# Optimization experiments

Hardware: AMD Instinct MI355X
Metric: run time of the kernel (lower is better)

## Reference

```python
import jax, jax.numpy as jnp
import numpy as np

EPS = 1e-8


def setup_inputs() -> dict:
    key = jax.random.key(0)
    k1, k2, k3, k4 = jax.random.split(key, 4)
    N, D, P, H = 8192, 512, 128, 128
    x1 = jax.random.normal(k1, (N, D), dtype=jnp.float32)
    proj_w1 = jax.random.normal(k2, (D, D), dtype=jnp.float32) * (1.0 / np.sqrt(D))
    proj_w2 = jax.random.normal(k3, (D, P), dtype=jnp.float32) * (1.0 / np.sqrt(D))
    gc_w = jax.random.normal(k4, (D, H), dtype=jnp.float32) * (1.0 / np.sqrt(D))
    gc_b = jnp.zeros((H,), dtype=jnp.float32)
    return {"x1": x1, "proj_w1": proj_w1, "proj_w2": proj_w2, "gc_w": gc_w, "gc_b": gc_b}


def _cosine_similarity(x):
    # torch.mm(x, x.T) / clamp(||x|| * ||x||.T, eps)
    w = jnp.sqrt(jnp.sum(x * x, axis=1, keepdims=True))  # [N,1]
    return (x @ x.T) / jnp.maximum(w * w.T, EPS)


def reference(x1, proj_w1, proj_w2, gc_w, gc_b):
    # projector: Linear(512,512,bias=False) -> ReLU -> Linear(512,P,bias=False)
    x_proj = jax.nn.relu(x1 @ proj_w1) @ proj_w2  # [N,P]
    # graph build is under @torch.no_grad(): dense fully-connected weighted graph
    A = jax.lax.stop_gradient(_cosine_similarity(x_proj))  # [N,N]
    N = x1.shape[0]
    # WGraphConv (DGL GraphConv w/ edge weights, norm='both'):
    # fully connected graph incl. self loops -> in_degree = N, norm = N^{-1/2} on both sides
    inv_n = jnp.asarray(1.0 / N, dtype=x1.dtype)
    h = x1 @ gc_w            # project first (D > H, cheaper)  [N,H]
    h = (A @ h) * inv_n      # weighted aggregate, symmetric degree norm
    return h + gc_b          # [N,H]
```

## Files before the change

kernel.cpp:

```cpp
#include <hip/hip_runtime.h>
#include <stdint.h>
#include <stddef.h>

typedef short s16x4 __attribute__((ext_vector_type(4)));
typedef short s16x8 __attribute__((ext_vector_type(8)));
typedef float f32x4 __attribute__((ext_vector_type(4)));

#define NN 8192
#define DD 512
#define PP 128
#define HH 128

__device__ __forceinline__ short f2bf(float f) {
  unsigned u = __builtin_bit_cast(unsigned, f);
  u = (u + 0x7fffu + ((u >> 16) & 1u)) >> 16;
  return (short)u;
}

__device__ __forceinline__ void async16(const void* g, void* l) {
  __builtin_amdgcn_global_load_lds(
      (const __attribute__((address_space(1))) unsigned int*)g,
      (__attribute__((address_space(3))) unsigned int*)l, 16, 0, 0);
}

template <int MF>
__device__ __forceinline__ void gemm_core(
    const short* __restrict__ A, long lda,
    const short* __restrict__ BT, long ldb,
    long rowBase, long colBase, int k0, int k1,
    short* As, short* Bs, f32x4 (*acc)[4]) {
  const int tid  = threadIdx.x;
  const int lane = tid & 63;
  const int wid  = tid >> 6;
  const int wr   = (wid >> 1) * (MF * 16);
  const int wc   = (wid & 1) * 64;
  const int srow = lane >> 3;
  const int skk  = (lane & 7) * 8;

  for (int k = k0; k < k1; k += 64) {
#pragma unroll
    for (int it = 0; it < MF; ++it) {
      int r = wid * (MF * 8) + it * 8;
      async16(A + (rowBase + r + srow) * lda + k + skk, As + r * 64);
    }
#pragma unroll
    for (int it = 0; it < 4; ++it) {
      int r = wid * 32 + it * 8;
      async16(BT + (colBase + r + srow) * ldb + k + skk, Bs + r * 64);
    }
    __syncthreads();
#pragma unroll
    for (int ks = 0; ks < 64; ks += 32) {
      s16x8 af[MF], bfv[4];
#pragma unroll
      for (int i = 0; i < MF; ++i)
        af[i]  = *(const s16x8*)(As + (wr + i * 16 + (lane & 15)) * 64 + ks + (lane >> 4) * 8);
#pragma unroll
      for (int i = 0; i < 4; ++i)
        bfv[i] = *(const s16x8*)(Bs + (wc + i * 16 + (lane & 15)) * 64 + ks + (lane >> 4) * 8);
#pragma unroll
      for (int mi = 0; mi < MF; ++mi)
#pragma unroll
        for (int ni = 0; ni < 4; ++ni)
          acc[mi][ni] = __builtin_amdgcn_mfma_f32_16x16x32_bf16(af[mi], bfv[ni], acc[mi][ni], 0, 0, 0);
    }
    __syncthreads();
  }
}

__global__ __launch_bounds__(256) void k_prep(
    const float* __restrict__ x1, const float* __restrict__ w1,
    const float* __restrict__ w2, const float* __restrict__ gcw,
    short* __restrict__ x1b, short* __restrict__ w1t,
    short* __restrict__ w2t, short* __restrict__ gcwt) {
  long b = blockIdx.x;
  int t = threadIdx.x;
  if (b < 4096) {
    long i = b * 256 + t;
    float4 v = ((const float4*)x1)[i];
    s16x4 o;
    o[0] = f2bf(v.x); o[1] = f2bf(v.y); o[2] = f2bf(v.z); o[3] = f2bf(v.w);
    *(s16x4*)(x1b + i * 4) = o;
  } else if (b < 4096 + 1024) {
    long i = (b - 4096) * 256 + t;
    int n = (int)(i >> 9), k = (int)(i & 511);
    w1t[i] = f2bf(w1[(long)k * DD + n]);
  } else if (b < 4096 + 1024 + 256) {
    long i = (b - 5120) * 256 + t;
    int n = (int)(i >> 9), k = (int)(i & 511);
    w2t[i] = f2bf(w2[(long)k * PP + n]);
  } else {
    long i = (b - 5376) * 256 + t;
    int n = (int)(i >> 9), k = (int)(i & 511);
    gcwt[i] = f2bf(gcw[(long)k * HH + n]);
  }
}

__global__ __launch_bounds__(256) void k_g13(const short* __restrict__ x1b,
                                             const short* __restrict__ w1t,
                                             const short* __restrict__ gcwt,
                                             short* __restrict__ Y,
                                             short* __restrict__ hT) {
  __shared__ __align__(16) short As[64 * 64];
  __shared__ __align__(16) short Bs[128 * 64];
  __shared__ __align__(16) short hs[128][66];
  f32x4 acc[2][4];
  f32x4 z = {0.f, 0.f, 0.f, 0.f};
#pragma unroll
  for (int i = 0; i < 2; ++i)
#pragma unroll
    for (int j = 0; j < 4; ++j) acc[i][j] = z;
  const int bx = blockIdx.x;
  const int lane = threadIdx.x & 63, wid = threadIdx.x >> 6;
  const int wr = (wid >> 1) * 32, wc = (wid & 1) * 64;
  if (bx < 512) {
    long rowBase = (long)(bx >> 2) * 64;
    long colBase = (long)(bx & 3) * 128;
    gemm_core<2>(x1b, DD, w1t, DD, rowBase, colBase, 0, DD, As, Bs, acc);
#pragma unroll
    for (int mi = 0; mi < 2; ++mi)
#pragma unroll
      for (int ni = 0; ni < 4; ++ni)
#pragma unroll
        for (int r = 0; r < 4; ++r) {
          long m = rowBase + wr + mi * 16 + ((lane >> 4) << 2) + r;
          long n = colBase + wc + ni * 16 + (lane & 15);
          float v = acc[mi][ni][r];
          Y[m * DD + n] = f2bf(v > 0.f ? v : 0.f);
        }
  } else {
    long rowBase = (long)(bx - 512) * 64;
    gemm_core<2>(x1b, DD, gcwt, DD, rowBase, 0, 0, DD, As, Bs, acc);
#pragma unroll
    for (int mi = 0; mi < 2; ++mi)
#pragma unroll
      for (int ni = 0; ni < 4; ++ni)
#pragma unroll
        for (int r = 0; r < 4; ++r) {
          int mloc = wr + mi * 16 + ((lane >> 4) << 2) + r;
          int n = wc + ni * 16 + (lane & 15);
          hs[n][mloc] = f2bf(acc[mi][ni][r]);
        }
    __syncthreads();
    int t = threadIdx.x;
    int h = t >> 1, m0 = (t & 1) * 32;
#pragma unroll
    for (int j0 = 0; j0 < 32; j0 += 8) {
      s16x8 o;
#pragma unroll
      for (int u = 0; u < 8; ++u) o[u] = hs[h][m0 + j0 + u];
      *(s16x8*)(hT + (long)h * NN + rowBase + m0 + j0) = o;
    }
  }
}

__global__ __launch_bounds__(256) void k_g2(const short* __restrict__ Y,
                                            const short* __restrict__ w2t,
                                            short* __restrict__ xp,
                                            short* __restrict__ xpT,
                                            float* __restrict__ invnw) {
  __shared__ __align__(16) short As[64 * 64];
  __shared__ __align__(16) short Bs[128 * 64];
  __shared__ float xs[64][129];
  __shared__ float invw_s[64];
  f32x4 acc[2][4];
  f32x4 z = {0.f, 0.f, 0.f, 0.f};
#pragma unroll
  for (int i = 0; i < 2; ++i)
#pragma unroll
    for (int j = 0; j < 4; ++j) acc[i][j] = z;
  long rowBase = (long)blockIdx.x * 64;
  gemm_core<2>(Y, DD, w2t, DD, rowBase, 0, 0, DD, As, Bs, acc);
  const int lane = threadIdx.x & 63, wid = threadIdx.x >> 6;
  const int wr = (wid >> 1) * 32, wc = (wid & 1) * 64;
#pragma unroll
  for (int mi = 0; mi < 2; ++mi)
#pragma unroll
    for (int ni = 0; ni < 4; ++ni)
#pragma unroll
      for (int r = 0; r < 4; ++r)
        xs[wr + mi * 16 + ((lane >> 4) << 2) + r][wc + ni * 16 + (lane & 15)] = acc[mi][ni][r];
  __syncthreads();
  int t = threadIdx.x;
  if (t < 64) {
    float s = 0.f;
#pragma unroll 8
    for (int i = 0; i < 128; ++i) { int c = (t + i) & 127; float v = xs[t][c]; s += v * v; }
    float nr = sqrtf(s);
    invnw[rowBase + t] = 1.f / (8192.f * nr);
    invw_s[t] = 1.f / nr;
  }
  __syncthreads();
#pragma unroll
  for (int i = 0; i < 4; ++i) {
    int seg = i * 256 + t;
    int r = seg >> 4, c0 = (seg & 15) * 8;
    s16x8 o;
#pragma unroll
    for (int u = 0; u < 8; ++u) o[u] = f2bf(xs[r][c0 + u]);
    *(s16x8*)(xp + (long)(rowBase + r) * PP + c0) = o;
  }
  int c = t >> 1, n0 = (t & 1) * 32;
#pragma unroll
  for (int j0 = 0; j0 < 32; j0 += 8) {
    s16x8 o;
#pragma unroll
    for (int u = 0; u < 8; ++u) {
      int n = n0 + j0 + u;
      o[u] = f2bf(xs[n][c] * invw_s[n]);
    }
    *(s16x8*)(xpT + (long)c * NN + rowBase + n0 + j0) = o;
  }
}

__global__ __launch_bounds__(256) void k_ge(const short* __restrict__ xpT,
                                            const short* __restrict__ hT,
                                            float* __restrict__ Gp) {
  __shared__ __align__(16) short As[128 * 64];
  __shared__ __align__(16) short Bs[128 * 64];
  f32x4 acc[4][4];
  f32x4 z = {0.f, 0.f, 0.f, 0.f};
#pragma unroll
  for (int i = 0; i < 4; ++i)
#pragma unroll
    for (int j = 0; j < 4; ++j) acc[i][j] = z;
  int s = blockIdx.x;
  gemm_core<4>(xpT, NN, hT, NN, 0, 0, s * 128, s * 128 + 128, As, Bs, acc);
  const int lane = threadIdx.x & 63, wid = threadIdx.x >> 6;
  const int wr = (wid >> 1) * 64, wc = (wid & 1) * 64;
#pragma unroll
  for (int mi = 0; mi < 4; ++mi)
#pragma unroll
    for (int ni = 0; ni < 4; ++ni)
#pragma unroll
      for (int r = 0; r < 4; ++r) {
        int m = wr + mi * 16 + ((lane >> 4) << 2) + r;
        int n = wc + ni * 16 + (lane & 15);
        Gp[(long)s * (PP * HH) + m * HH + n] = acc[mi][ni][r];
      }
}

__global__ __launch_bounds__(256) void k_red(const float* __restrict__ Gp,
                                             short* __restrict__ GT) {
  int i = blockIdx.x * 256 + threadIdx.x;
  float s = 0.f;
#pragma unroll 8
  for (int j = 0; j < 64; ++j) s += Gp[j * (PP * HH) + i];
  int p = i >> 7, h = i & 127;
  GT[h * PP + p] = f2bf(s);
}

__global__ __launch_bounds__(256) void k_gf(const short* __restrict__ xp,
                                            const short* __restrict__ GT,
                                            const float* __restrict__ invnw,
                                            const float* __restrict__ gcb,
                                            float* __restrict__ out) {
  __shared__ __align__(16) short As[64 * 64];
  __shared__ __align__(16) short Bs[128 * 64];
  f32x4 acc[2][4];
  f32x4 z = {0.f, 0.f, 0.f, 0.f};
#pragma unroll
  for (int i = 0; i < 2; ++i)
#pragma unroll
    for (int j = 0; j < 4; ++j) acc[i][j] = z;
  long rowBase = (long)blockIdx.x * 64;
  gemm_core<2>(xp, PP, GT, PP, rowBase, 0, 0, PP, As, Bs, acc);
  const int lane = threadIdx.x & 63, wid = threadIdx.x >> 6;
  const int wr = (wid >> 1) * 32, wc = (wid & 1) * 64;
#pragma unroll
  for (int mi = 0; mi < 2; ++mi)
#pragma unroll
    for (int ni = 0; ni < 4; ++ni)
#pragma unroll
      for (int r = 0; r < 4; ++r) {
        long m = rowBase + wr + mi * 16 + ((lane >> 4) << 2) + r;
        int n = wc + ni * 16 + (lane & 15);
        out[m * HH + n] = acc[mi][ni][r] * invnw[m] + gcb[n];
      }
}

extern "C" void kernel_launch(void* const* d_in, const int* in_sizes, int n_in,
                              void* d_out, int out_size, void* d_ws, size_t ws_size,
                              hipStream_t stream) {
  const float* x1  = (const float*)d_in[0];
  const float* w1  = (const float*)d_in[1];
  const float* w2  = (const float*)d_in[2];
  const float* gcw = (const float*)d_in[3];
  const float* gcb = (const float*)d_in[4];
  float* out = (float*)d_out;

  char* ws = (char*)d_ws;
  size_t off = 0;
  auto alloc = [&](size_t bytes) -> char* {
    char* p = ws + off;
    off += (bytes + 255) & ~(size_t)255;
    return p;
  };
  short* x1b  = (short*)alloc((size_t)NN * DD * 2);
  short* w1t  = (short*)alloc((size_t)DD * DD * 2);
  short* w2t  = (short*)alloc((size_t)PP * DD * 2);
  short* gcwt = (short*)alloc((size_t)HH * DD * 2);
  short* Y    = (short*)alloc((size_t)NN * DD * 2);
  short* xp   = (short*)alloc((size_t)NN * PP * 2);
  short* xpT  = (short*)alloc((size_t)NN * PP * 2);
  short* hT   = (short*)alloc((size_t)NN * HH * 2);
  float* invnw = (float*)alloc((size_t)NN * 4);
  float* Gp   = (float*)alloc((size_t)64 * PP * HH * 4);
  short* GT   = (short*)alloc((size_t)PP * HH * 2);

  hipLaunchKernelGGL(k_prep, dim3(5632), dim3(256), 0, stream,
                     x1, w1, w2, gcw, x1b, w1t, w2t, gcwt);
  hipLaunchKernelGGL(k_g13, dim3(640), dim3(256), 0, stream, x1b, w1t, gcwt, Y, hT);
  hipLaunchKernelGGL(k_g2, dim3(128), dim3(256), 0, stream, Y, w2t, xp, xpT, invnw);
  hipLaunchKernelGGL(k_ge, dim3(64), dim3(256), 0, stream, xpT, hT, Gp);
  hipLaunchKernelGGL(k_red, dim3(64), dim3(256), 0, stream, Gp, GT);
  hipLaunchKernelGGL(k_gf, dim3(128), dim3(256), 0, stream, xp, GT, invnw, gcb, out);
}
```

Before: 53.86 us.

## Double-buffer LDS tiles in shared GEMM core to overlap loads with MFMA

Replaces the single-buffered GEMM mainloop with a two-stage LDS ping-pong. The next K-tile's async global-to-LDS copies are issued before the MFMA work on the current tile. The goal is to hide global load latency behind compute instead of stalling at a barrier each iteration. It raises LDS use per block (up to 64KB in k_ge), which can lower occupancy, and the short-K kernels only run two iterations, so they gain little.

```diff
diff --git a/kernel.cpp b/kernel.cpp
--- a/kernel.cpp
+++ b/kernel.cpp
@@ -24,11 +24,12 @@
 }
 
 template <int MF>
-__device__ __forceinline__ void gemm_core(
+__device__ __forceinline__ void gemm_core2(
     const short* __restrict__ A, long lda,
     const short* __restrict__ BT, long ldb,
     long rowBase, long colBase, int k0, int k1,
-    short* As, short* Bs, f32x4 (*acc)[4]) {
+    short* As0, short* Bs0, short* As1, short* Bs1,
+    f32x4 (*acc)[4]) {
   const int tid  = threadIdx.x;
   const int lane = tid & 63;
   const int wid  = tid >> 6;
@@ -37,27 +38,33 @@
   const int srow = lane >> 3;
   const int skk  = (lane & 7) * 8;
 
+#define STAGE_(AS, BS, KK)                                                    \
+  do {                                                                        \
+    _Pragma("unroll")                                                         \
+    for (int it = 0; it < MF; ++it) {                                         \
+      int r = wid * (MF * 8) + it * 8;                                        \
+      async16(A + (rowBase + r + srow) * lda + (KK) + skk, (AS) + r * 64);    \
+    }                                                                         \
+    _Pragma("unroll")                                                         \
+    for (int it = 0; it < 4; ++it) {                                          \
+      int r = wid * 32 + it * 8;                                              \
+      async16(BT + (colBase + r + srow) * ldb + (KK) + skk, (BS) + r * 64);   \
+    }                                                                         \
+  } while (0)
+
+  STAGE_(As0, Bs0, k0);
+  __syncthreads();
   for (int k = k0; k < k1; k += 64) {
-#pragma unroll
-    for (int it = 0; it < MF; ++it) {
-      int r = wid * (MF * 8) + it * 8;
-      async16(A + (rowBase + r + srow) * lda + k + skk, As + r * 64);
-    }
-#pragma unroll
-    for (int it = 0; it < 4; ++it) {
-      int r = wid * 32 + it * 8;
-      async16(BT + (colBase + r + srow) * ldb + k + skk, Bs + r * 64);
-    }
-    __syncthreads();
+    if (k + 64 < k1) STAGE_(As1, Bs1, k + 64);
 #pragma unroll
     for (int ks = 0; ks < 64; ks += 32) {
       s16x8 af[MF], bfv[4];
 #pragma unroll
       for (int i = 0; i < MF; ++i)
-        af[i]  = *(const s16x8*)(As + (wr + i * 16 + (lane & 15)) * 64 + ks + (lane >> 4) * 8);
+        af[i]  = *(const s16x8*)(As0 + (wr + i * 16 + (lane & 15)) * 64 + ks + (lane >> 4) * 8);
 #pragma unroll
       for (int i = 0; i < 4; ++i)
-        bfv[i] = *(const s16x8*)(Bs + (wc + i * 16 + (lane & 15)) * 64 + ks + (lane >> 4) * 8);
+        bfv[i] = *(const s16x8*)(Bs0 + (wc + i * 16 + (lane & 15)) * 64 + ks + (lane >> 4) * 8);
 #pragma unroll
       for (int mi = 0; mi < MF; ++mi)
 #pragma unroll
@@ -65,7 +72,16 @@
           acc[mi][ni] = __builtin_amdgcn_mfma_f32_16x16x32_bf16(af[mi], bfv[ni], acc[mi][ni], 0, 0, 0);
     }
     __syncthreads();
-  }
+    short* t0 = As0; As0 = As1; As1 = t0;
+    short* t1 = Bs0; Bs0 = Bs1; Bs1 = t1;
+  }
+#undef STAGE_
+}
+
+__device__ __forceinline__ void zero_acc2(f32x4 (*acc)[4], int mf) {
+  f32x4 z = {0.f, 0.f, 0.f, 0.f};
+  for (int i = 0; i < mf; ++i)
+    for (int j = 0; j < 4; ++j) acc[i][j] = z;
 }
 
 __global__ __launch_bounds__(256) void k_prep(
@@ -101,22 +117,20 @@
                                              const short* __restrict__ gcwt,
                                              short* __restrict__ Y,
                                              short* __restrict__ hT) {
-  __shared__ __align__(16) short As[64 * 64];
-  __shared__ __align__(16) short Bs[128 * 64];
-  __shared__ __align__(16) short hs[128][66];
+  __shared__ __align__(16) char smem[49152];
+  short* As0 = (short*)smem;
+  short* As1 = (short*)(smem + 8192);
+  short* Bs0 = (short*)(smem + 16384);
+  short* Bs1 = (short*)(smem + 32768);
   f32x4 acc[2][4];
-  f32x4 z = {0.f, 0.f, 0.f, 0.f};
-#pragma unroll
-  for (int i = 0; i < 2; ++i)
-#pragma unroll
-    for (int j = 0; j < 4; ++j) acc[i][j] = z;
+  zero_acc2(acc, 2);
   const int bx = blockIdx.x;
   const int lane = threadIdx.x & 63, wid = threadIdx.x >> 6;
   const int wr = (wid >> 1) * 32, wc = (wid & 1) * 64;
   if (bx < 512) {
     long rowBase = (long)(bx >> 2) * 64;
     long colBase = (long)(bx & 3) * 128;
-    gemm_core<2>(x1b, DD, w1t, DD, rowBase, colBase, 0, DD, As, Bs, acc);
+    gemm_core2<2>(x1b, DD, w1t, DD, rowBase, colBase, 0, DD, As0, Bs0, As1, Bs1, acc);
 #pragma unroll
     for (int mi = 0; mi < 2; ++mi)
 #pragma unroll
@@ -130,16 +144,17 @@
         }
   } else {
     long rowBase = (long)(bx - 512) * 64;
-    gemm_core<2>(x1b, DD, gcwt, DD, rowBase, 0, 0, DD, As, Bs, acc);
+    gemm_core2<2>(x1b, DD, gcwt, DD, rowBase, 0, 0, DD, As0, Bs0, As1, Bs1, acc);
+    short (*hs)[66] = (short(*)[66])smem;
 #pragma unroll
     for (int mi = 0; mi < 2; ++mi)
 #pragma unroll
       for (int ni = 0; ni < 4; ++ni)
 #pragma unroll
         for (int r = 0; r < 4; ++r) {
-          int mloc = wr + mi * 16 + ((lane >> 4) << 2) + r;
+          int m = wr + mi * 16 + ((lane >> 4) << 2) + r;
           int n = wc + ni * 16 + (lane & 15);
-          hs[n][mloc] = f2bf(acc[mi][ni][r]);
+          hs[n][m] = f2bf(acc[mi][ni][r]);
         }
     __syncthreads();
     int t = threadIdx.x;
@@ -159,20 +174,19 @@
                                             short* __restrict__ xp,
                                             short* __restrict__ xpT,
                                             float* __restrict__ invnw) {
-  __shared__ __align__(16) short As[64 * 64];
-  __shared__ __align__(16) short Bs[128 * 64];
-  __shared__ float xs[64][129];
+  __shared__ __align__(16) char smem[49152];
+  short* As0 = (short*)smem;
+  short* As1 = (short*)(smem + 8192);
+  short* Bs0 = (short*)(smem + 16384);
+  short* Bs1 = (short*)(smem + 32768);
   __shared__ float invw_s[64];
   f32x4 acc[2][4];
-  f32x4 z = {0.f, 0.f, 0.f, 0.f};
-#pragma unroll
-  for (int i = 0; i < 2; ++i)
-#pragma unroll
-    for (int j = 0; j < 4; ++j) acc[i][j] = z;
+  zero_acc2(acc, 2);
   long rowBase = (long)blockIdx.x * 64;
-  gemm_core<2>(Y, DD, w2t, DD, rowBase, 0, 0, DD, As, Bs, acc);
+  gemm_core2<2>(Y, DD, w2t, DD, rowBase, 0, 0, DD, As0, Bs0, As1, Bs1, acc);
   const int lane = threadIdx.x & 63, wid = threadIdx.x >> 6;
   const int wr = (wid >> 1) * 32, wc = (wid & 1) * 64;
+  float (*xs)[129] = (float(*)[129])smem;
 #pragma unroll
   for (int mi = 0; mi < 2; ++mi)
 #pragma unroll
@@ -216,16 +230,15 @@
 __global__ __launch_bounds__(256) void k_ge(const short* __restrict__ xpT,
                                             const short* __restrict__ hT,
                                             float* __restrict__ Gp) {
-  __shared__ __align__(16) short As[128 * 64];
-  __shared__ __align__(16) short Bs[128 * 64];
+  __shared__ __align__(16) char smem[65536];
+  short* As0 = (short*)smem;
+  short* As1 = (short*)(smem + 16384);
+  short* Bs0 = (short*)(smem + 32768);
+  short* Bs1 = (short*)(smem + 49152);
   f32x4 acc[4][4];
-  f32x4 z = {0.f, 0.f, 0.f, 0.f};
-#pragma unroll
-  for (int i = 0; i < 4; ++i)
-#pragma unroll
-    for (int j = 0; j < 4; ++j) acc[i][j] = z;
+  zero_acc2(acc, 4);
   int s = blockIdx.x;
-  gemm_core<4>(xpT, NN, hT, NN, 0, 0, s * 128, s * 128 + 128, As, Bs, acc);
+  gemm_core2<4>(xpT, NN, hT, NN, 0, 0, s * 128, s * 128 + 128, As0, Bs0, As1, Bs1, acc);
   const int lane = threadIdx.x & 63, wid = threadIdx.x >> 6;
   const int wr = (wid >> 1) * 64, wc = (wid & 1) * 64;
 #pragma unroll
@@ -255,16 +268,15 @@
                                             const float* __restrict__ invnw,
                                             const float* __restrict__ gcb,
                                             float* __restrict__ out) {
-  __shared__ __align__(16) short As[64 * 64];
-  __shared__ __align__(16) short Bs[128 * 64];
+  __shared__ __align__(16) char smem[49152];
+  short* As0 = (short*)smem;
+  short* As1 = (short*)(smem + 8192);
+  short* Bs0 = (short*)(smem + 16384);
+  short* Bs1 = (short*)(smem + 32768);
   f32x4 acc[2][4];
-  f32x4 z = {0.f, 0.f, 0.f, 0.f};
-#pragma unroll
-  for (int i = 0; i < 2; ++i)
-#pragma unroll
-    for (int j = 0; j < 4; ++j) acc[i][j] = z;
+  zero_acc2(acc, 2);
   long rowBase = (long)blockIdx.x * 64;
-  gemm_core<2>(xp, PP, GT, PP, rowBase, 0, 0, PP, As, Bs, acc);
+  gemm_core2<2>(xp, PP, GT, PP, rowBase, 0, 0, PP, As0, Bs0, As1, Bs1, acc);
   const int lane = threadIdx.x & 63, wid = threadIdx.x >> 6;
   const int wr = (wid >> 1) * 32, wc = (wid & 1) * 64;
 #pragma unroll
```

Measured after the change: 51.77 us. -3.9%, faster.
